# Optimization experiments

Hardware: AMD Instinct MI355X
Metric: run time of the kernel (lower is better)

Reference implementation:

```python
import jax, jax.numpy as jnp
import numpy as np

B, S, D, H = 2, 2048, 1024, 16
DK = D // H  # 64


def setup_inputs() -> dict:
    key = jax.random.key(0)
    k0, k1, k2, k3, k4, k5, k6 = jax.random.split(key, 7)
    scale = 0.02
    return {
        "q": jax.random.normal(k0, (B, S, D), dtype=jnp.float32),
        "k": jax.random.normal(k1, (B, S, D), dtype=jnp.float32),
        "v": jax.random.normal(k2, (B, S, D), dtype=jnp.float32),
        # per-head Q/K projection weights (n_head separate Linear layers, bias=False)
        "Wq": jax.random.normal(k3, (H, D, DK), dtype=jnp.float32) * scale,
        "Wk": jax.random.normal(k4, (H, D, DK), dtype=jnp.float32) * scale,
        # shared V projection (the same v_layer object is reused for every head)
        "Wv": jax.random.normal(k5, (D, DK), dtype=jnp.float32) * scale,
        # output projection fc: d_v -> d_model, bias=False
        "Wo": jax.random.normal(k6, (DK, D), dtype=jnp.float32) * scale,
    }


def reference(q, k, v, Wq, Wk, Wv, Wo):
    d_k = Wq.shape[-1]
    # batched per-head projections (replaces the Python loop over heads)
    qs = jnp.einsum("bsd,hdk->bhsk", q, Wq)          # [B,H,S,DK]
    ks = jnp.einsum("bsd,hdk->bhsk", k, Wk)          # [B,H,S,DK]
    vs = jnp.einsum("bsd,dk->bsk", v, Wv)            # [B,S,DK] shared across heads
    scores = jnp.einsum("bhsk,bhtk->bhst", qs, ks) / jnp.sqrt(
        jnp.asarray(d_k, dtype=jnp.float32)
    )                                                 # [B,H,S,S]
    attn = jax.nn.softmax(scores, axis=-1)            # [B,H,S,S]; dropout = identity (eval)
    heads = jnp.einsum("bhst,btk->bhsk", attn, vs)    # [B,H,S,DK]
    head = heads.mean(axis=1)                         # mean over heads, not concat
    attn_mean = attn.mean(axis=1)                     # [B,S,S]
    out = jnp.einsum("bsk,kd->bsd", head, Wo)         # [B,S,D]; dropout = identity
    return (out, attn_mean)
```

## Files before the change

### kernel.cpp

```cpp
#include <hip/hip_runtime.h>

#define B_ 2
#define S_ 2048
#define D_ 1024
#define H_ 16
#define DK_ 64

typedef __bf16 bf8 __attribute__((ext_vector_type(8)));
typedef float f4 __attribute__((ext_vector_type(4)));
typedef unsigned short u16x8 __attribute__((ext_vector_type(8)));

__device__ __forceinline__ unsigned short f2bf_bits(float f) {
  unsigned int u = __float_as_uint(f);
  return (unsigned short)((u + 0x7fffu + ((u >> 16) & 1u)) >> 16);
}

__device__ __forceinline__ bf8 pack_bf8(f4 lo, f4 hi) {
  u16x8 u;
  u[0] = f2bf_bits(lo[0]); u[1] = f2bf_bits(lo[1]);
  u[2] = f2bf_bits(lo[2]); u[3] = f2bf_bits(lo[3]);
  u[4] = f2bf_bits(hi[0]); u[5] = f2bf_bits(hi[1]);
  u[6] = f2bf_bits(hi[2]); u[7] = f2bf_bits(hi[3]);
  union { u16x8 u; bf8 b; } x; x.u = u; return x.b;
}

__device__ __forceinline__ bf8 ldb(const unsigned short* p) {
  return *reinterpret_cast<const bf8*>(p);
}

__device__ __forceinline__ void stage16(const void* g, void* l) {
  __builtin_amdgcn_global_load_lds(
      (const __attribute__((address_space(1))) void*)g,
      (__attribute__((address_space(3))) void*)l, 16, 0, 0);
}

#define MFMA(a, b, c) __builtin_amdgcn_mfma_f32_16x16x32_bf16((a), (b), (c), 0, 0, 0)

__global__ void k_prep(const float* __restrict__ q, const float* __restrict__ k,
                       const float* __restrict__ wq, const float* __restrict__ wk,
                       const float* __restrict__ wv, const float* __restrict__ wo,
                       unsigned short* __restrict__ qb, unsigned short* __restrict__ kb,
                       unsigned short* __restrict__ wqt, unsigned short* __restrict__ wkt,
                       unsigned short* __restrict__ wvt, unsigned short* __restrict__ wot) {
  __shared__ float tl[64 * 65];
  int bid = blockIdx.x, tid = threadIdx.x;
  const int rr = tid >> 6, cc = tid & 63;
  if (bid < 4096) {
    int which = bid >> 11;
    long i = ((long)(bid & 2047) * 256 + tid) * 8;
    const float* src = which ? k : q;
    unsigned short* dst = which ? kb : qb;
    f4 lo = *reinterpret_cast<const f4*>(src + i);
    f4 hi = *reinterpret_cast<const f4*>(src + i + 4);
    *reinterpret_cast<bf8*>(dst + i) = pack_bf8(lo, hi);
  } else if (bid < 4352) {
    int blk = bid - 4096;
    int h = blk >> 4, d0 = (blk & 15) * 64;
    for (int m = 0; m < 2; ++m) {
      const float* src = m ? wk : wq;
      unsigned short* dst = m ? wkt : wqt;
      if (m) __syncthreads();
#pragma unroll
      for (int it = 0; it < 16; ++it) {
        int d = it * 4 + rr;
        tl[cc * 65 + d] = src[(long)h * 65536 + (d0 + d) * 64 + cc];
      }
      __syncthreads();
#pragma unroll
      for (int it = 0; it < 16; ++it) {
        int n = it * 4 + rr;
        dst[(long)h * 65536 + n * 1024 + d0 + cc] = f2bf_bits(tl[n * 65 + cc]);
      }
    }
  } else if (bid < 4368) {
    int d0 = (bid - 4352) * 64;
#pragma unroll
    for (int it = 0; it < 16; ++it) {
      int d = it * 4 + rr;
      tl[cc * 65 + d] = wv[(long)(d0 + d) * 64 + cc];
    }
    __syncthreads();
#pragma unroll
    for (int it = 0; it < 16; ++it) {
      int n = it * 4 + rr;
      wvt[(long)n * 1024 + d0 + cc] = f2bf_bits(tl[n * 65 + cc]);
    }
  } else {
    int d0 = (bid - 4368) * 64;
#pragma unroll
    for (int it = 0; it < 16; ++it) {
      int kk = it * 4 + rr;
      tl[cc * 65 + kk] = wo[(long)kk * 1024 + d0 + cc];
    }
    __syncthreads();
#pragma unroll
    for (int it = 0; it < 16; ++it) {
      int ddl = it * 4 + rr;
      wot[(long)(d0 + ddl) * 64 + cc] = f2bf_bits(tl[ddl * 65 + cc]);
    }
  }
}

__global__ __launch_bounds__(256) void k_qkpv(
    const unsigned short* __restrict__ qb, const unsigned short* __restrict__ kb,
    const unsigned short* __restrict__ wqt, const unsigned short* __restrict__ wkt,
    unsigned short* __restrict__ qsb, unsigned short* __restrict__ ksb,
    const float* __restrict__ v, const unsigned short* __restrict__ wvt,
    float* __restrict__ pv) {
  __shared__ unsigned short lds[24576];
  const int tid = threadIdx.x, wave = tid >> 6, lane = tid & 63;
  const int l15 = lane & 15, quad = lane >> 4;

  if (blockIdx.x >= 512) {
    const int bid2 = blockIdx.x - 512;
    const int rg = bid2 & 63, kc = bid2 >> 6;
    const int row0 = rg * 64 + wave * 16;
    const float* arow = v + (long)(row0 + l15) * D_ + kc * 256 + quad * 8;
    const unsigned short* wbase = wvt + kc * 256 + quad * 8;
    f4 acc[4];
    for (int i = 0; i < 4; ++i) acc[i] = f4{0.f, 0.f, 0.f, 0.f};
    for (int k0 = 0; k0 < 256; k0 += 32) {
      f4 alo = *reinterpret_cast<const f4*>(arow + k0);
      f4 ahi = *reinterpret_cast<const f4*>(arow + k0 + 4);
      bf8 a = pack_bf8(alo, ahi);
#pragma unroll
      for (int i = 0; i < 4; ++i) {
        bf8 bf = ldb(wbase + (long)(i * 16 + l15) * D_ + k0);
        acc[i] = MFMA(a, bf, acc[i]);
      }
    }
#pragma unroll
    for (int i = 0; i < 4; ++i)
#pragma unroll
      for (int r = 0; r < 4; ++r)
        pv[((long)kc * 4096 + row0 + quad * 4 + r) * 64 + i * 16 + l15] = acc[i][r];
    return;
  }

  const int n = blockIdx.x, xcd = n & 7, slot = n >> 3;
  const int which = xcd >> 2;
  const int m0 = (((xcd & 3) << 3) | (slot & 7)) * 128;
  const int n0 = (slot >> 3) * 128;
  const unsigned short* A = which ? kb : qb;
  const unsigned short* W = which ? wkt : wqt;
  unsigned short* C = which ? ksb : qsb;
  const float scale = which ? 1.0f : 0.18033688011112042f;
  const int wr = wave >> 1, wc = wave & 1;

  f4 acc[4][4];
#pragma unroll
  for (int i = 0; i < 4; ++i)
#pragma unroll
    for (int j = 0; j < 4; ++j) acc[i][j] = f4{0.f, 0.f, 0.f, 0.f};

  const int sl15 = tid & 15, squad = (tid >> 4) & 3, st = tid >> 6;
  const unsigned short* gA = A + (long)(m0 + st * 16 + sl15) * D_ + squad * 8;
  const unsigned short* gB = W + (long)(n0 + st * 16 + sl15) * D_ + squad * 8;

  stage16(gA, lds + tid * 8);
  stage16(gA + 64 * D_, lds + 2048 + tid * 8);
  stage16(gB, lds + 4096 + tid * 8);
  stage16(gB + 64 * D_, lds + 6144 + tid * 8);
  stage16(gA + 32, lds + 8192 + tid * 8);
  stage16(gA + 64 * D_ + 32, lds + 10240 + tid * 8);
  stage16(gB + 32, lds + 12288 + tid * 8);
  stage16(gB + 64 * D_ + 32, lds + 14336 + tid * 8);
  asm volatile("s_waitcnt vmcnt(4)" ::: "memory");
  __builtin_amdgcn_s_barrier();
  int rd = 0;

  for (int it = 0; it < 32; ++it) {
    if (it + 2 < 32) {
      const int k2 = (it + 2) * 32;
      int wb = rd + 2; if (wb >= 3) wb -= 3;
      unsigned short* nb = lds + wb * 8192;
      stage16(gA + k2, nb + tid * 8);
      stage16(gA + 64 * D_ + k2, nb + 2048 + tid * 8);
      stage16(gB + k2, nb + 4096 + tid * 8);
      stage16(gB + 64 * D_ + k2, nb + 6144 + tid * 8);
    }
    const unsigned short* base = lds + rd * 8192;
    __builtin_amdgcn_s_setprio(1);
    bf8 aF[4], bF[4];
#pragma unroll
    for (int mi = 0; mi < 4; ++mi)
      aF[mi] = ldb(base + (wr * 4 + mi) * 512 + lane * 8);
#pragma unroll
    for (int ni = 0; ni < 4; ++ni)
      bF[ni] = ldb(base + 4096 + (wc * 4 + ni) * 512 + lane * 8);
#pragma unroll
    for (int mi = 0; mi < 4; ++mi)
#pragma unroll
      for (int ni = 0; ni < 4; ++ni)
        acc[mi][ni] = MFMA(aF[mi], bF[ni], acc[mi][ni]);
    __builtin_amdgcn_s_setprio(0);
    if (it + 1 < 32) {
      if (it + 2 < 32)
        asm volatile("s_waitcnt vmcnt(4)" ::: "memory");
      else
        asm volatile("s_waitcnt vmcnt(0)" ::: "memory");
      __builtin_amdgcn_s_barrier();
      rd = (rd + 1 == 3) ? 0 : rd + 1;
    }
  }
#pragma unroll
  for (int mi = 0; mi < 4; ++mi)
#pragma unroll
    for (int r = 0; r < 4; ++r) {
      long row = m0 + wr * 64 + mi * 16 + quad * 4 + r;
#pragma unroll
      for (int ni = 0; ni < 4; ++ni)
        C[row * D_ + n0 + wc * 64 + ni * 16 + l15] = f2bf_bits(acc[mi][ni][r] * scale);
    }
}

__global__ __launch_bounds__(512) void k_denomv(
    const unsigned short* __restrict__ qsb, const unsigned short* __restrict__ ksb,
    float* __restrict__ recip,
    const float* __restrict__ pv, unsigned short* __restrict__ vst) {
  __shared__ unsigned short lds[16384];
  const int tid = threadIdx.x, wave = tid >> 6, lane = tid & 63;
  const int l15 = lane & 15, quad = lane >> 4;

  if (blockIdx.x >= 512) {
    int e = (blockIdx.x - 512) * 512 + tid;
    int t = e & 2047, dk = (e >> 11) & 63, b = e >> 17;
    long row = (long)b * S_ + t;
    float s = pv[row * 64 + dk] + pv[(4096 + row) * 64 + dk] +
              pv[(8192 + row) * 64 + dk] + pv[(12288 + row) * 64 + dk];
    vst[e] = f2bf_bits(s);
    return;
  }

  const int n = blockIdx.x, xcd = n & 7, slot = n >> 3;
  const int b = xcd >> 2;
  const int h = ((xcd & 3) << 2) | (slot & 3);
  const int stile = slot >> 2;
  const int s0 = stile * 128 + wave * 16;

  const unsigned short* qrow = qsb + ((long)(b * S_) + s0 + l15) * D_ + h * 64 + quad * 8;
  bf8 a0 = ldb(qrow);
  bf8 a1 = ldb(qrow + 32);

  const int sl15 = tid & 15, squad = (tid >> 4) & 3, stt = (tid >> 6) & 7;
  const unsigned short* g0 =
      ksb + ((long)(b * S_) + stt * 16 + sl15) * D_ + h * 64 + squad * 8;

  stage16(g0, lds + tid * 8);
  stage16(g0 + 32, lds + 4096 + tid * 8);
  asm volatile("s_waitcnt vmcnt(0)" ::: "memory");
  __builtin_amdgcn_s_barrier();
  int cur = 0;

  f4 sum = f4{0.f, 0.f, 0.f, 0.f};
  for (int it = 0; it < 16; ++it) {
    if (it + 1 < 16) {
      const unsigned short* gn = g0 + (long)(it + 1) * 128 * D_;
      unsigned short* nb = lds + (cur ^ 1) * 8192;
      stage16(gn, nb + tid * 8);
      stage16(gn + 32, nb + 4096 + tid * 8);
    }
    const unsigned short* base = lds + cur * 8192;
    __builtin_amdgcn_s_setprio(1);
#pragma unroll
    for (int tt = 0; tt < 8; ++tt) {
      bf8 b0 = ldb(base + tt * 512 + lane * 8);
      bf8 b1 = ldb(base + 4096 + tt * 512 + lane * 8);
      f4 d = f4{0.f, 0.f, 0.f, 0.f};
      d = MFMA(a0, b0, d);
      d = MFMA(a1, b1, d);
#pragma unroll
      for (int r = 0; r < 4; ++r) sum[r] += __builtin_amdgcn_exp2f(d[r]);
    }
    __builtin_amdgcn_s_setprio(0);
    if (it + 1 < 16) {
      asm volatile("s_waitcnt vmcnt(0)" ::: "memory");
      __builtin_amdgcn_s_barrier();
      cur ^= 1;
    }
  }
#pragma unroll
  for (int m = 1; m < 16; m <<= 1) {
#pragma unroll
    for (int r = 0; r < 4; ++r) sum[r] += __shfl_xor(sum[r], m, 64);
  }
  if (l15 == 0) {
    float* rp = recip + (long)(b * H_ + h) * S_ + s0 + quad * 4;
#pragma unroll
    for (int r = 0; r < 4; ++r) rp[r] = 1.0f / (16.0f * sum[r]);
  }
}

__global__ __launch_bounds__(512) void k_attn(
    const unsigned short* __restrict__ qsb, const unsigned short* __restrict__ ksb,
    const float* __restrict__ recip, float* __restrict__ am) {
  __shared__ unsigned short lds[16384];
  const int tid = threadIdx.x, wave = tid >> 6, lane = tid & 63;
  const int l15 = lane & 15, quad = lane >> 4;
  const int n = blockIdx.x, xcd = n & 7, slot = n >> 3;
  const int b = xcd >> 2;
  const int tchunk = ((xcd & 1) << 3) | (slot & 7);
  const int stile = (((xcd >> 1) & 1) << 3) | (slot >> 3);
  const int s0 = stile * 128 + wave * 16;
  const int t0c = tchunk * 128;

  f4 acc[8];
#pragma unroll
  for (int tt = 0; tt < 8; ++tt) acc[tt] = f4{0.f, 0.f, 0.f, 0.f};

  const unsigned short* qbase = qsb + ((long)(b * S_) + s0 + l15) * D_ + quad * 8;
  const int sl15 = tid & 15, squad = (tid >> 4) & 3, stt = (tid >> 6) & 7;
  const unsigned short* g0 =
      ksb + ((long)(b * S_) + t0c + stt * 16 + sl15) * D_ + squad * 8;
  const float* rbase = recip + (long)(b * H_) * S_ + s0 + quad * 4;

  stage16(g0, lds + tid * 8);
  stage16(g0 + 32, lds + 4096 + tid * 8);
  bf8 a0 = ldb(qbase);
  bf8 a1 = ldb(qbase + 32);
  f4 rp = *reinterpret_cast<const f4*>(rbase);
  asm volatile("s_waitcnt vmcnt(0)" ::: "memory");
  __builtin_amdgcn_s_barrier();
  int cur = 0;

  for (int h = 0; h < H_; ++h) {
    bf8 a0n, a1n;
    f4 rpn;
    if (h + 1 < H_) {
      a0n = ldb(qbase + (h + 1) * 64);
      a1n = ldb(qbase + (h + 1) * 64 + 32);
      rpn = *reinterpret_cast<const f4*>(rbase + (long)(h + 1) * S_);
      __builtin_amdgcn_sched_barrier(0);
      const unsigned short* gn = g0 + (h + 1) * 64;
      unsigned short* nb = lds + (cur ^ 1) * 8192;
      stage16(gn, nb + tid * 8);
      stage16(gn + 32, nb + 4096 + tid * 8);
    }
    const unsigned short* base = lds + cur * 8192;
    __builtin_amdgcn_s_setprio(1);
#pragma unroll
    for (int tt = 0; tt < 8; ++tt) {
      bf8 b0 = ldb(base + tt * 512 + lane * 8);
      bf8 b1 = ldb(base + 4096 + tt * 512 + lane * 8);
      f4 d = f4{0.f, 0.f, 0.f, 0.f};
      d = MFMA(a0, b0, d);
      d = MFMA(a1, b1, d);
#pragma unroll
      for (int r = 0; r < 4; ++r) acc[tt][r] += rp[r] * __builtin_amdgcn_exp2f(d[r]);
    }
    __builtin_amdgcn_s_setprio(0);
    if (h + 1 < H_) {
      asm volatile("s_waitcnt vmcnt(0)" ::: "memory");
      __builtin_amdgcn_s_barrier();
      cur ^= 1;
      a0 = a0n;
      a1 = a1n;
      rp = rpn;
    }
  }
  float* obase = am + ((long)b * S_ + s0 + quad * 4) * S_ + t0c + l15;
#pragma unroll
  for (int tt = 0; tt < 8; ++tt)
#pragma unroll
    for (int r = 0; r < 4; ++r) obase[(long)r * S_ + tt * 16] = acc[tt][r];
}

__global__ __launch_bounds__(256) void k_hpart(
    const float* __restrict__ am, const unsigned short* __restrict__ vst,
    float* __restrict__ ph) {
  const int tid = threadIdx.x, wave = tid >> 6, lane = tid & 63;
  const int l15 = lane & 15, quad = lane >> 4;
  const int rg = blockIdx.x, kc = blockIdx.y;
  const int row0 = rg * 64 + wave * 16;
  const int b = row0 >> 11;
  const float* arow = am + (long)(row0 + l15) * S_ + kc * 512 + quad * 8;
  const unsigned short* vb = vst + (long)b * DK_ * S_ + kc * 512 + quad * 8;
  f4 acc[4];
  for (int i = 0; i < 4; ++i) acc[i] = f4{0.f, 0.f, 0.f, 0.f};
  for (int t0 = 0; t0 < 512; t0 += 32) {
    f4 alo = *reinterpret_cast<const f4*>(arow + t0);
    f4 ahi = *reinterpret_cast<const f4*>(arow + t0 + 4);
    bf8 a = pack_bf8(alo, ahi);
#pragma unroll
    for (int i = 0; i < 4; ++i) {
      bf8 bf = ldb(vb + (long)(i * 16 + l15) * S_ + t0);
      acc[i] = MFMA(a, bf, acc[i]);
    }
  }
#pragma unroll
  for (int i = 0; i < 4; ++i)
#pragma unroll
    for (int r = 0; r < 4; ++r)
      ph[((long)kc * 4096 + row0 + quad * 4 + r) * 64 + i * 16 + l15] = acc[i][r];
}

__global__ void k_hred(const float* __restrict__ ph, unsigned short* __restrict__ headb) {
  int e = blockIdx.x * 256 + threadIdx.x;
  float s = ph[e] + ph[e + 4096 * 64] + ph[e + 2 * 4096 * 64] + ph[e + 3 * 4096 * 64];
  headb[e] = f2bf_bits(s);
}

__global__ __launch_bounds__(256) void k_out(
    const unsigned short* __restrict__ head, const unsigned short* __restrict__ wot,
    float* __restrict__ out) {
  const int tid = threadIdx.x, wave = tid >> 6, lane = tid & 63;
  const int l15 = lane & 15, quad = lane >> 4;
  const int dchunk = blockIdx.x, stile = blockIdx.y, b = blockIdx.z;
  const int s0 = stile * 64 + wave * 16;
  const int n0 = dchunk * 128;
  const unsigned short* hrow = head + ((long)b * S_ + s0 + l15) * DK_ + quad * 8;
  bf8 a0 = ldb(hrow);
  bf8 a1 = ldb(hrow + 32);
  const unsigned short* wb = wot + quad * 8;
  float* obase = out + ((long)b * S_ + s0 + quad * 4) * D_ + n0 + l15;
#pragma unroll
  for (int i = 0; i < 8; ++i) {
    const unsigned short* wp = wb + (long)(n0 + i * 16 + l15) * DK_;
    bf8 b0 = ldb(wp);
    bf8 b1 = ldb(wp + 32);
    f4 d = f4{0.f, 0.f, 0.f, 0.f};
    d = MFMA(a0, b0, d);
    d = MFMA(a1, b1, d);
#pragma unroll
    for (int r = 0; r < 4; ++r) obase[(long)r * D_ + i * 16] = d[r];
  }
}

extern "C" void kernel_launch(void* const* d_in, const int* in_sizes, int n_in,
                              void* d_out, int out_size, void* d_ws, size_t ws_size,
                              hipStream_t stream) {
  const float* q  = (const float*)d_in[0];
  const float* k  = (const float*)d_in[1];
  const float* v  = (const float*)d_in[2];
  const float* Wq = (const float*)d_in[3];
  const float* Wk = (const float*)d_in[4];
  const float* Wv = (const float*)d_in[5];
  const float* Wo = (const float*)d_in[6];

  float* out = (float*)d_out;
  float* am  = out + (long)B_ * S_ * D_;

  unsigned short* qsb  = (unsigned short*)d_ws;
  unsigned short* ksb  = qsb + 4194304;
  unsigned short* wqt  = ksb + 4194304;
  unsigned short* wkt  = wqt + 1048576;
  unsigned short* wvt  = wkt + 1048576;
  unsigned short* wot  = wvt + 65536;
  unsigned short* vst  = wot + 65536;
  unsigned short* headb= vst + 262144;
  float* recip = (float*)(headb + 262144);

  unsigned short* qb = (unsigned short*)am;
  unsigned short* kb = qb + 4194304;
  float* part = out;

  k_prep<<<4384, 256, 0, stream>>>(q, k, Wq, Wk, Wv, Wo, qb, kb, wqt, wkt, wvt, wot);
  k_qkpv<<<768, 256, 0, stream>>>(qb, kb, wqt, wkt, qsb, ksb, v, wvt, part);
  k_denomv<<<1024, 512, 0, stream>>>(qsb, ksb, recip, part, vst);
  k_attn<<<512, 512, 0, stream>>>(qsb, ksb, recip, am);
  k_hpart<<<dim3(64, 4), 256, 0, stream>>>(am, vst, part);
  k_hred<<<1024, 256, 0, stream>>>(part, headb);
  k_out<<<dim3(8, 32, 2), 256, 0, stream>>>(headb, wot, out);
}
```

Before: 234.3 us.

## Fuse attn@V head product into attention kernel with atomic accumulation

```diff
diff --git a/kernel.cpp b/kernel.cpp
--- a/kernel.cpp
+++ b/kernel.cpp
@@ -217,11 +217,16 @@
 __global__ __launch_bounds__(512) void k_denomv(
     const unsigned short* __restrict__ qsb, const unsigned short* __restrict__ ksb,
     float* __restrict__ recip,
-    const float* __restrict__ pv, unsigned short* __restrict__ vst) {
+    const float* __restrict__ pv, unsigned short* __restrict__ vst,
+    float* __restrict__ headf) {
   __shared__ unsigned short lds[16384];
   const int tid = threadIdx.x, wave = tid >> 6, lane = tid & 63;
   const int l15 = lane & 15, quad = lane >> 4;
 
+  if (blockIdx.x >= 1024) {
+    headf[(blockIdx.x - 1024) * 512 + tid] = 0.f;
+    return;
+  }
   if (blockIdx.x >= 512) {
     int e = (blockIdx.x - 512) * 512 + tid;
     int t = e & 2047, dk = (e >> 11) & 63, b = e >> 17;
@@ -293,7 +298,8 @@
 
 __global__ __launch_bounds__(512) void k_attn(
     const unsigned short* __restrict__ qsb, const unsigned short* __restrict__ ksb,
-    const float* __restrict__ recip, float* __restrict__ am) {
+    const float* __restrict__ recip, float* __restrict__ am,
+    const unsigned short* __restrict__ vst, float* __restrict__ headf) {
   __shared__ unsigned short lds[16384];
   const int tid = threadIdx.x, wave = tid >> 6, lane = tid & 63;
   const int l15 = lane & 15, quad = lane >> 4;
@@ -363,54 +369,55 @@
   for (int tt = 0; tt < 8; ++tt)
 #pragma unroll
     for (int r = 0; r < 4; ++r) obase[(long)r * S_ + tt * 16] = acc[tt][r];
-}
-
-__global__ __launch_bounds__(256) void k_hpart(
-    const float* __restrict__ am, const unsigned short* __restrict__ vst,
-    float* __restrict__ ph) {
-  const int tid = threadIdx.x, wave = tid >> 6, lane = tid & 63;
-  const int l15 = lane & 15, quad = lane >> 4;
-  const int rg = blockIdx.x, kc = blockIdx.y;
-  const int row0 = rg * 64 + wave * 16;
-  const int b = row0 >> 11;
-  const float* arow = am + (long)(row0 + l15) * S_ + kc * 512 + quad * 8;
-  const unsigned short* vb = vst + (long)b * DK_ * S_ + kc * 512 + quad * 8;
-  f4 acc[4];
-  for (int i = 0; i < 4; ++i) acc[i] = f4{0.f, 0.f, 0.f, 0.f};
-  for (int t0 = 0; t0 < 512; t0 += 32) {
-    f4 alo = *reinterpret_cast<const f4*>(arow + t0);
-    f4 ahi = *reinterpret_cast<const f4*>(arow + t0 + 4);
-    bf8 a = pack_bf8(alo, ahi);
-#pragma unroll
-    for (int i = 0; i < 4; ++i) {
-      bf8 bf = ldb(vb + (long)(i * 16 + l15) * S_ + t0);
-      acc[i] = MFMA(a, bf, acc[i]);
-    }
-  }
-#pragma unroll
-  for (int i = 0; i < 4; ++i)
+
+  __syncthreads();
+  {
+    const int prowb = wave * 16 + quad * 4;
+#pragma unroll
+    for (int tt = 0; tt < 8; ++tt)
+#pragma unroll
+      for (int r = 0; r < 4; ++r)
+        lds[(prowb + r) * 128 + tt * 16 + l15] = f2bf_bits(acc[tt][r]);
+  }
+  __syncthreads();
+  const unsigned short* prd = lds + (wave * 16 + l15) * 128 + quad * 8;
+  bf8 paF[4];
+#pragma unroll
+  for (int kk = 0; kk < 4; ++kk) paF[kk] = ldb(prd + kk * 32);
+  const unsigned short* vbb = vst + ((long)b * DK_ + l15) * S_ + t0c + quad * 8;
+  f4 pacc[4];
+#pragma unroll
+  for (int ni = 0; ni < 4; ++ni) pacc[ni] = f4{0.f, 0.f, 0.f, 0.f};
+#pragma unroll
+  for (int ni = 0; ni < 4; ++ni)
+#pragma unroll
+    for (int kk = 0; kk < 4; ++kk) {
+      bf8 bf = ldb(vbb + (long)(ni * 16) * S_ + kk * 32);
+      pacc[ni] = MFMA(paF[kk], bf, pacc[ni]);
+    }
+  const long rbase2 = (long)b * S_ + stile * 128 + wave * 16 + quad * 4;
+#pragma unroll
+  for (int ni = 0; ni < 4; ++ni)
 #pragma unroll
     for (int r = 0; r < 4; ++r)
-      ph[((long)kc * 4096 + row0 + quad * 4 + r) * 64 + i * 16 + l15] = acc[i][r];
-}
-
-__global__ void k_hred(const float* __restrict__ ph, unsigned short* __restrict__ headb) {
-  int e = blockIdx.x * 256 + threadIdx.x;
-  float s = ph[e] + ph[e + 4096 * 64] + ph[e + 2 * 4096 * 64] + ph[e + 3 * 4096 * 64];
-  headb[e] = f2bf_bits(s);
+      atomicAdd(headf + (rbase2 + r) * 64 + ni * 16 + l15, pacc[ni][r]);
 }
 
 __global__ __launch_bounds__(256) void k_out(
-    const unsigned short* __restrict__ head, const unsigned short* __restrict__ wot,
+    const float* __restrict__ headf, const unsigned short* __restrict__ wot,
     float* __restrict__ out) {
   const int tid = threadIdx.x, wave = tid >> 6, lane = tid & 63;
   const int l15 = lane & 15, quad = lane >> 4;
   const int dchunk = blockIdx.x, stile = blockIdx.y, b = blockIdx.z;
   const int s0 = stile * 64 + wave * 16;
   const int n0 = dchunk * 128;
-  const unsigned short* hrow = head + ((long)b * S_ + s0 + l15) * DK_ + quad * 8;
-  bf8 a0 = ldb(hrow);
-  bf8 a1 = ldb(hrow + 32);
+  const float* hrow = headf + ((long)b * S_ + s0 + l15) * DK_ + quad * 8;
+  f4 h0lo = *reinterpret_cast<const f4*>(hrow);
+  f4 h0hi = *reinterpret_cast<const f4*>(hrow + 4);
+  f4 h1lo = *reinterpret_cast<const f4*>(hrow + 32);
+  f4 h1hi = *reinterpret_cast<const f4*>(hrow + 36);
+  bf8 a0 = pack_bf8(h0lo, h0hi);
+  bf8 a1 = pack_bf8(h1lo, h1hi);
   const unsigned short* wb = wot + quad * 8;
   float* obase = out + ((long)b * S_ + s0 + quad * 4) * D_ + n0 + l15;
 #pragma unroll
@@ -453,12 +460,11 @@
   unsigned short* qb = (unsigned short*)am;
   unsigned short* kb = qb + 4194304;
   float* part = out;
+  float* headf = (float*)wqt;
 
   k_prep<<<4384, 256, 0, stream>>>(q, k, Wq, Wk, Wv, Wo, qb, kb, wqt, wkt, wvt, wot);
   k_qkpv<<<768, 256, 0, stream>>>(qb, kb, wqt, wkt, qsb, ksb, v, wvt, part);
-  k_denomv<<<1024, 512, 0, stream>>>(qsb, ksb, recip, part, vst);
-  k_attn<<<512, 512, 0, stream>>>(qsb, ksb, recip, am);
-  k_hpart<<<dim3(64, 4), 256, 0, stream>>>(am, vst, part);
-  k_hred<<<1024, 256, 0, stream>>>(part, headb);
-  k_out<<<dim3(8, 32, 2), 256, 0, stream>>>(headb, wot, out);
-}
+  k_denomv<<<1536, 512, 0, stream>>>(qsb, ksb, recip, part, vst, headf);
+  k_attn<<<512, 512, 0, stream>>>(qsb, ksb, recip, am, vst, headf);
+  k_out<<<dim3(8, 32, 2), 256, 0, stream>>>(headf, wot, out);
+}
```

After: 232.8 us. Within noise of the previous version (-0.7%).
